# Kernel optimization log

Hardware: AMD Instinct MI355X
Metric: run time of the kernel (lower is better)

Reference implementation:

```python
import jax, jax.numpy as jnp
import numpy as np

B, N, C, D = 2, 6, 64, 40
FH, FW = 12, 33
IMG_H, IMG_W = 384, 1056
NX, NY, NZ = 100, 100, 4
LOWER = np.array([-50.0, -50.0, -10.0], np.float32)   # xbound[0], ybound[0], zbound[0]
DXV = np.array([1.0, 1.0, 5.0], np.float32)           # voxel sizes


def _conv(x, w, pad):
    return jax.lax.conv_general_dilated(x, w, (1, 1), [(pad, pad), (pad, pad)],
                                        dimension_numbers=('NCHW', 'OIHW', 'NCHW'))


def _bn(x, s, b):
    return x * s[None, :, None, None] + b[None, :, None, None]


def _se(x, w1, b1, w2, b2):
    m = x.mean((2, 3))                                   # global avg pool -> (B, C)
    g = jax.nn.sigmoid(jax.nn.silu(m @ w1.T + b1) @ w2.T + b2)
    return x * g[:, :, None, None]


def _frustum():
    ds = jnp.arange(4.0, 44.0, 1.0)                      # (D,) depth bins
    xs = jnp.linspace(0.0, IMG_W - 1.0, FW)
    ys = jnp.linspace(0.0, IMG_H - 1.0, FH)
    f = jnp.stack(jnp.broadcast_arrays(xs[None, None, :], ys[None, :, None], ds[:, None, None]), -1)
    return f.reshape(-1, 3)                              # (D*FH*FW, 3) in (x_px, y_px, depth)


def reference(feats, rots, trans, intrinsics, nw1, bn1s, bn1b, se1w1, se1b1, se1w2, se1b2,
              nw2, bn2s, bn2b, dhw, dhb, chw, chb, bcw1, bcs1, bcb1, bcsw1, bcsb1, bcsw2,
              bcsb2, bcw2, bcs2, bcb2, dw1, ds1, db1, dw2, db2):
    BN = B * N
    # ---- CamEncoderV2 neck + heads (backbone 1280ch@1/32 features given directly) ----
    x = jax.nn.silu(_bn(_conv(feats, nw1, 0), bn1s, bn1b))
    x = _se(x, se1w1, se1b1, se1w2, se1b2)
    x = jax.nn.silu(_bn(_conv(x, nw2, 1), bn2s, bn2b))
    depth = jax.nn.softmax(_conv(x, dhw, 0) + dhb[None, :, None, None], axis=1)  # (BN, D, FH, FW)
    ctx = _conv(x, chw, 0) + chb[None, :, None, None]                            # (BN, C, FH, FW)
    # ---- geometry: pixel frustum -> ego-frame points ----
    rots_f = rots.reshape(BN, 3, 3)
    trans_f = trans.reshape(BN, 3)
    K = intrinsics.reshape(BN, 3, 3)
    pts = _frustum()                                     # (P0, 3), P0 = D*FH*FW
    d = pts[:, 2]
    fx, fy = K[:, 0, 0][:, None], K[:, 1, 1][:, None]
    cx, cy = K[:, 0, 2][:, None], K[:, 1, 2][:, None]
    cam = jnp.stack([(pts[None, :, 0] - cx) * d[None, :] / fx,
                     (pts[None, :, 1] - cy) * d[None, :] / fy,
                     jnp.broadcast_to(d[None, :], (BN, d.shape[0]))], -1)        # (BN, P0, 3)
    geom = jnp.einsum('bij,bpj->bpi', rots_f, cam) + trans_f[:, None, :]
    geom = geom.reshape(B, -1, 3)                        # (B, N*P0, 3)
    # ---- lift: outer product context x depth ----
    ff = (ctx[:, None, :, :, :] * depth[:, :, None, :, :])                       # (BN, D, C, FH, FW)
    ff = ff.transpose(0, 1, 3, 4, 2).reshape(B, -1, C)                           # (B, N*P0, C)
    # ---- splat: voxel pooling (scatter-add into BEV grid) ----
    idx = jnp.floor((geom - jnp.asarray(LOWER)) / jnp.asarray(DXV)).astype(jnp.int32)
    valid = jnp.all((idx >= 0) & (idx < jnp.array([NX, NY, NZ])), axis=-1)
    sid = idx[..., 2] * (NX * NY) + idx[..., 0] * NY + idx[..., 1]
    sid = jnp.where(valid, sid, 0)
    ffm = ff * valid[..., None]
    pooled = jax.vmap(lambda f, i: jax.ops.segment_sum(f, i, num_segments=NZ * NX * NY))(ffm, sid)
    bev = pooled.reshape(B, NZ, NX, NY, C).transpose(0, 1, 4, 2, 3).reshape(B, NZ * C, NX, NY)
    # ---- BEVCompressorV2 (residual conv-SE-conv) ----
    h = jax.nn.relu(_bn(_conv(bev, bcw1, 1), bcs1, bcb1))
    h = _se(h, bcsw1, bcsb1, bcsw2, bcsb2)
    h = jax.nn.relu(_bn(_conv(h, bcw2, 1), bcs2, bcb2))
    bev = bev + h
    # ---- decoder ----
    h = jax.nn.relu(_bn(_conv(bev, dw1, 1), ds1, db1))
    out = _conv(h, dw2, 0) + db2[None, :, None, None]    # (B, nz*num_classes, NX, NY)
    return out.reshape(B, 4, NZ, NX, NY)


def setup_inputs():
    f32 = jnp.float32
    ks = jax.random.split(jax.random.key(0), 16)
    feats = jax.random.normal(ks[0], (B * N, 1280, FH, FW), f32) * 0.5
    # cam->ego: z_cam -> x_ego, -x_cam -> y_ego, -y_cam -> z_ego, plus per-camera yaw
    Rbase = np.array([[0., 0., 1.], [-1., 0., 0.], [0., -1., 0.]], np.float32)
    yaw = np.deg2rad(np.arange(N) * 60.0).astype(np.float32)
    c, s = np.cos(yaw), np.sin(yaw)
    Rz = np.zeros((N, 3, 3), np.float32)
    Rz[:, 0, 0] = c; Rz[:, 0, 1] = -s; Rz[:, 1, 0] = s; Rz[:, 1, 1] = c; Rz[:, 2, 2] = 1.0
    rots = jnp.asarray(np.broadcast_to(np.einsum('nij,jk->nik', Rz, Rbase), (B, N, 3, 3)).copy())
    trans = jax.random.normal(ks[1], (B, N, 3), f32) * 1.0
    K = np.array([[800., 0., 528.], [0., 800., 192.], [0., 0., 1.]], np.float32)
    intrinsics = jnp.asarray(np.broadcast_to(K, (B, N, 3, 3)).copy())

    def w(k, shape, fan_in):
        return jax.random.normal(k, shape, f32) * np.float32(np.sqrt(2.0 / fan_in))

    kk = jax.random.split(ks[2], 16)
    return dict(
        feats=feats, rots=rots, trans=trans, intrinsics=intrinsics,
        nw1=w(kk[0], (256, 1280, 1, 1), 1280), bn1s=jnp.ones(256, f32), bn1b=jnp.zeros(256, f32),
        se1w1=w(kk[1], (32, 256), 256), se1b1=jnp.zeros(32, f32),
        se1w2=w(kk[2], (256, 32), 32), se1b2=jnp.zeros(256, f32),
        nw2=w(kk[3], (256, 256, 3, 3), 2304), bn2s=jnp.ones(256, f32), bn2b=jnp.zeros(256, f32),
        dhw=w(kk[4], (40, 256, 1, 1), 256), dhb=jnp.zeros(40, f32),
        chw=w(kk[5], (64, 256, 1, 1), 256), chb=jnp.zeros(64, f32),
        bcw1=w(kk[6], (256, 256, 3, 3), 2304), bcs1=jnp.ones(256, f32), bcb1=jnp.zeros(256, f32),
        bcsw1=w(kk[7], (16, 256), 256), bcsb1=jnp.zeros(16, f32),
        bcsw2=w(kk[8], (256, 16), 16), bcsb2=jnp.zeros(256, f32),
        bcw2=w(kk[9], (256, 256, 3, 3), 2304), bcs2=jnp.ones(256, f32), bcb2=jnp.zeros(256, f32),
        dw1=w(kk[10], (128, 256, 3, 3), 2304), ds1=jnp.ones(128, f32), db1=jnp.zeros(128, f32),
        dw2=w(kk[11], (16, 128, 1, 1), 128), db2=jnp.zeros(16, f32),
    )
```

## Files before the change

kernel.cpp:

```cpp
#include <hip/hip_runtime.h>
#include <hip/hip_bf16.h>
#include <cmath>


typedef __attribute__((ext_vector_type(8))) short short8;
typedef __attribute__((ext_vector_type(4))) float floatx4;
typedef __hip_bfloat16 hb;

__device__ __forceinline__ float sigf(float x){ return 1.0f/(1.0f+expf(-x)); }
__device__ __forceinline__ float siluf(float x){ return x*sigf(x); }
__device__ __forceinline__ void split2(float v, hb* h, hb* l){
  hb hv = __float2bfloat16(v);
  *h = hv; *l = __float2bfloat16(v - __bfloat162float(hv));
}

__global__ __launch_bounds__(256) void k_trans_feats(
    const float* __restrict__ feats, hb* __restrict__ Fh, hb* __restrict__ Fl)
{
  __shared__ float tile[64][65];
  int n = blockIdx.z;
  int p0 = blockIdx.x*64;
  int c0 = blockIdx.y*64;
  int tid = threadIdx.x;
  int tr = tid >> 6;
  int tc = tid & 63;
  #pragma unroll
  for (int it=0; it<16; ++it){
    int ci = c0 + it*4 + tr;
    int p = p0 + tc;
    float v = 0.f;
    if (p < 396) v = feats[((size_t)n*1280 + ci)*396 + p];
    tile[it*4+tr][tc] = v;
  }
  __syncthreads();
  #pragma unroll
  for (int it=0; it<16; ++it){
    int pl = it*4 + tr;
    int p = p0 + pl;
    if (p < 396){
      hb hv, lv; split2(tile[tc][pl], &hv, &lv);
      size_t o = ((size_t)n*396 + p)*1280 + c0 + tc;
      Fh[o] = hv; Fl[o] = lv;
    }
  }
}

__global__ __launch_bounds__(256) void k_wpack1(
    const float* __restrict__ W, hb* __restrict__ Wph, hb* __restrict__ Wpl)
{
  int i = blockIdx.x*256 + threadIdx.x;
  if (i >= 40*16*512) return;
  int j = i & 7;
  int lane = (i>>3) & 63;
  int t2 = i >> 9;
  int nb = t2 & 15;
  int kb = t2 >> 4;
  int ci = kb*32 + (lane>>4)*8 + j;
  int co = nb*16 + (lane&15);
  hb hv, lv; split2(W[(size_t)co*1280 + ci], &hv, &lv);
  Wph[i] = hv; Wpl[i] = lv;
}

__global__ __launch_bounds__(256) void k_wpack(
    const float* __restrict__ W, hb* __restrict__ Wph, hb* __restrict__ Wpl, int NB)
{
  int i = blockIdx.x*256 + threadIdx.x;
  int total = 9*8*NB*512;
  if (i >= total) return;
  int j = i & 7;
  int t1 = i >> 3;
  int lane = t1 & 63;
  int t2 = t1 >> 6;
  int nb = t2 % NB;
  int t3 = t2 / NB;
  int kb = t3 & 7;
  int tap = t3 >> 3;
  int ci = kb*32 + (lane>>4)*8 + j;
  int co = nb*16 + (lane&15);
  hb hv, lv; split2(W[(size_t)co*2304 + ci*9 + tap], &hv, &lv);
  Wph[i] = hv; Wpl[i] = lv;
}

__global__ __launch_bounds__(256) void k_wpackT(
    const float* __restrict__ W, hb* __restrict__ Wph, hb* __restrict__ Wpl, int NB)
{
  int i = blockIdx.x*256 + threadIdx.x;
  int total = 9*8*NB*512;
  if (i >= total) return;
  int j = i & 7;
  int t1 = i >> 3;
  int lane = t1 & 63;
  int t2 = t1 >> 6;
  int nb = t2 % NB;
  int t3 = t2 / NB;
  int tap = t3 % 9;
  int kb = t3 / 9;
  int ci = kb*32 + (lane>>4)*8 + j;
  int co = nb*16 + (lane&15);
  hb hv, lv; split2(W[(size_t)co*2304 + ci*9 + tap], &hv, &lv);
  Wph[i] = hv; Wpl[i] = lv;
}

__global__ __launch_bounds__(256) void k_mfma_gemm1(
    const hb* __restrict__ Fh, const hb* __restrict__ Fl,
    const hb* __restrict__ Wph, const hb* __restrict__ Wpl,
    const float* __restrict__ bns, const float* __restrict__ bnb,
    float* __restrict__ out)
{
  __shared__ short8 lbh[256], lbl[256];
  int tid = threadIdx.x;
  int wv = tid >> 6, lane = tid & 63;
  int cog = blockIdx.y;
  int Pbase = blockIdx.x*128 + wv*32;
  int m = lane & 15, q = lane >> 4;
  int P0 = Pbase + m;      if (P0 > 4751) P0 = 4751;
  int P1 = Pbase + 16 + m; if (P1 > 4751) P1 = 4751;
  size_t rA0 = (size_t)P0*160 + q;
  size_t rA1 = (size_t)P1*160 + q;
  const short8* gAh = (const short8*)(const void*)Fh;
  const short8* gAl = (const short8*)(const void*)Fl;
  const short8* gWh = (const short8*)(const void*)Wph;
  const short8* gWl = (const short8*)(const void*)Wpl;
  size_t sb = (size_t)(cog*4 + wv)*64 + lane;
  floatx4 acc[2][4];
  #pragma unroll
  for (int i=0;i<2;++i)
    #pragma unroll
    for (int j=0;j<4;++j) acc[i][j] = (floatx4)(0.f);
  short8 ph = gWh[sb], pw = gWl[sb];
  short8 cah0 = gAh[rA0], cal0 = gAl[rA0], cah1 = gAh[rA1], cal1 = gAl[rA1];
  for (int kb=0; kb<40; ++kb){
    __syncthreads();
    lbh[tid] = ph; lbl[tid] = pw;
    int nx = (kb+1 < 40) ? kb+1 : 39;
    ph = gWh[(size_t)nx*1024 + sb]; pw = gWl[(size_t)nx*1024 + sb];
    __syncthreads();
    short8 nah0 = gAh[rA0 + (size_t)nx*4];
    short8 nal0 = gAl[rA0 + (size_t)nx*4];
    short8 nah1 = gAh[rA1 + (size_t)nx*4];
    short8 nal1 = gAl[rA1 + (size_t)nx*4];
    #pragma unroll
    for (int nb=0; nb<4; ++nb){
      short8 bh = lbh[nb*64 + lane];
      short8 bl = lbl[nb*64 + lane];
      acc[0][nb] = __builtin_amdgcn_mfma_f32_16x16x32_bf16(cah0, bh, acc[0][nb], 0,0,0);
      acc[0][nb] = __builtin_amdgcn_mfma_f32_16x16x32_bf16(cah0, bl, acc[0][nb], 0,0,0);
      acc[0][nb] = __builtin_amdgcn_mfma_f32_16x16x32_bf16(cal0, bh, acc[0][nb], 0,0,0);
      acc[1][nb] = __builtin_amdgcn_mfma_f32_16x16x32_bf16(cah1, bh, acc[1][nb], 0,0,0);
      acc[1][nb] = __builtin_amdgcn_mfma_f32_16x16x32_bf16(cah1, bl, acc[1][nb], 0,0,0);
      acc[1][nb] = __builtin_amdgcn_mfma_f32_16x16x32_bf16(cal1, bh, acc[1][nb], 0,0,0);
    }
    cah0 = nah0; cal0 = nal0; cah1 = nah1; cal1 = nal1;
  }
  int n16 = lane & 15;
  #pragma unroll
  for (int mg=0; mg<2; ++mg){
    #pragma unroll
    for (int nb=0; nb<4; ++nb){
      int co = cog*64 + nb*16 + n16;
      float s = bns[co], bv = bnb[co];
      #pragma unroll
      for (int r=0; r<4; ++r){
        int P = Pbase + mg*16 + q*4 + r;
        if (P < 4752) out[(size_t)P*256 + co] = siluf(acc[mg][nb][r]*s + bv);
      }
    }
  }
}

__global__ __launch_bounds__(256) void k_meanN(
    const float* __restrict__ x1, float* __restrict__ mean)
{
  int n = blockIdx.x; int c = threadIdx.x;
  float s = 0.f;
  for (int p=0; p<396; ++p) s += x1[((size_t)n*396+p)*256 + c];
  mean[n*256+c] = s*(1.f/396.f);
}

__global__ __launch_bounds__(256) void k_se_fc(
    const float* __restrict__ mean, const float* __restrict__ w1, const float* __restrict__ b1,
    const float* __restrict__ w2, const float* __restrict__ b2, float* __restrict__ g, int H)
{
  __shared__ float m[256];
  __shared__ float h[32];
  int n = blockIdx.x; int t = threadIdx.x;
  m[t] = mean[n*256 + t];
  __syncthreads();
  if (t < H){
    float s = b1[t];
    for (int c=0; c<256; ++c) s += m[c]*w1[t*256+c];
    h[t] = siluf(s);
  }
  __syncthreads();
  float s = b2[t];
  for (int j=0; j<H; ++j) s += h[j]*w2[t*H+j];
  g[n*256+t] = sigf(s);
}

__global__ __launch_bounds__(256) void k_topad(
    const float* __restrict__ x1, const float* __restrict__ g,
    hb* __restrict__ Xh, hb* __restrict__ Xl)
{
  int y = blockIdx.x;
  int n = blockIdx.y;
  int c = threadIdx.x;
  float gc = g[n*256+c];
  for (int xx=0; xx<35; ++xx){
    float v = 0.f;
    if (y>=1 && y<=12 && xx>=1 && xx<=33)
      v = x1[((size_t)n*396 + (y-1)*33 + (xx-1))*256 + c]*gc;
    hb hv, lv; split2(v, &hv, &lv);
    size_t o = (((size_t)n*14+y)*35+xx)*256 + c;
    Xh[o] = hv; Xl[o] = lv;
  }
}

__global__ __launch_bounds__(256) void k_conv3s_mfma(
    const hb* __restrict__ Xh, const hb* __restrict__ Xl,
    const hb* __restrict__ Wph, const hb* __restrict__ Wpl,
    const float* __restrict__ bns, const float* __restrict__ bnb,
    float* __restrict__ out)
{
  __shared__ short8 lbh[256], lbl[256];
  int tid = threadIdx.x;
  int wv = tid >> 6, lane = tid & 63;
  int cog = blockIdx.y;
  int Pbase = blockIdx.x*128 + wv*32;
  int m = lane & 15, q = lane >> 4;
  int P0 = Pbase + m;      if (P0 > 4751) P0 = 4751;
  int P1 = Pbase + 16 + m; if (P1 > 4751) P1 = 4751;
  int n0 = P0/396, pim0 = P0%396;
  int n1 = P1/396, pim1 = P1%396;
  size_t base0 = (size_t)((n0*14 + pim0/33)*35 + pim0%33)*32 + q;
  size_t base1 = (size_t)((n1*14 + pim1/33)*35 + pim1%33)*32 + q;
  const short8* gAh = (const short8*)(const void*)Xh;
  const short8* gAl = (const short8*)(const void*)Xl;
  const short8* gWh = (const short8*)(const void*)Wph;
  const short8* gWl = (const short8*)(const void*)Wpl;
  size_t sb = (size_t)(cog*4 + wv)*64 + lane;
  floatx4 acc[2][4];
  #pragma unroll
  for (int i=0;i<2;++i)
    #pragma unroll
    for (int j=0;j<4;++j) acc[i][j] = (floatx4)(0.f);
  short8 ph = gWh[sb], pw = gWl[sb];
  short8 cah0 = gAh[base0], cal0 = gAl[base0], cah1 = gAh[base1], cal1 = gAl[base1];
  for (int idx=0; idx<72; ++idx){
    __syncthreads();
    lbh[tid] = ph; lbl[tid] = pw;
    int nx = (idx+1 < 72) ? idx+1 : 71;
    ph = gWh[(size_t)nx*1024 + sb]; pw = gWl[(size_t)nx*1024 + sb];
    __syncthreads();
    int tap = nx >> 3, kb = nx & 7;
    int dy = (tap*11) >> 5;
    int dx = tap - dy*3;
    int ao = (dy*35+dx)*32 + kb*4;
    short8 nah0 = gAh[base0 + ao];
    short8 nal0 = gAl[base0 + ao];
    short8 nah1 = gAh[base1 + ao];
    short8 nal1 = gAl[base1 + ao];
    #pragma unroll
    for (int nb=0; nb<4; ++nb){
      short8 bh = lbh[nb*64 + lane];
      short8 bl = lbl[nb*64 + lane];
      acc[0][nb] = __builtin_amdgcn_mfma_f32_16x16x32_bf16(cah0, bh, acc[0][nb], 0,0,0);
      acc[0][nb] = __builtin_amdgcn_mfma_f32_16x16x32_bf16(cah0, bl, acc[0][nb], 0,0,0);
      acc[0][nb] = __builtin_amdgcn_mfma_f32_16x16x32_bf16(cal0, bh, acc[0][nb], 0,0,0);
      acc[1][nb] = __builtin_amdgcn_mfma_f32_16x16x32_bf16(cah1, bh, acc[1][nb], 0,0,0);
      acc[1][nb] = __builtin_amdgcn_mfma_f32_16x16x32_bf16(cah1, bl, acc[1][nb], 0,0,0);
      acc[1][nb] = __builtin_amdgcn_mfma_f32_16x16x32_bf16(cal1, bh, acc[1][nb], 0,0,0);
    }
    cah0 = nah0; cal0 = nal0; cah1 = nah1; cal1 = nal1;
  }
  int n16 = lane & 15;
  #pragma unroll
  for (int mg=0; mg<2; ++mg){
    #pragma unroll
    for (int r=0; r<4; ++r){
      int P = Pbase + mg*16 + q*4 + r;
      if (P < 4752){
        int nn = P/396, pim = P%396;
        #pragma unroll
        for (int nb=0; nb<4; ++nb){
          int co = cog*64 + nb*16 + n16;
          out[((size_t)nn*256+co)*396 + pim] = siluf(acc[mg][nb][r]*bns[co] + bnb[co]);
        }
      }
    }
  }
}

__global__ __launch_bounds__(256) void k_heads(
    const float* __restrict__ x, const float* __restrict__ dhw, const float* __restrict__ dhb,
    const float* __restrict__ chw, const float* __restrict__ chb,
    float* __restrict__ dep, float* __restrict__ ctx2)
{
  int p = blockIdx.x*256 + threadIdx.x;
  int co = blockIdx.y; int n = blockIdx.z;
  if (p >= 396) return;
  const float* xb = x + (size_t)n*256*396 + p;
  const float* w = (co < 40) ? (dhw + (size_t)co*256) : (chw + (size_t)(co-40)*256);
  float acc = 0.f;
  for (int ci=0; ci<256; ++ci) acc += xb[(size_t)ci*396] * w[ci];
  if (co < 40) dep[((size_t)n*40+co)*396 + p] = acc + dhb[co];
  else { int c = co-40; ctx2[((size_t)n*396+p)*64 + c] = acc + chb[c]; }
}

__global__ __launch_bounds__(256) void k_softmax40(float* __restrict__ dep)
{
  int i = blockIdx.x*256 + threadIdx.x;
  if (i >= 12*396) return;
  int n = i/396, p = i%396;
  float* base = dep + (size_t)n*40*396 + p;
  float mx = -1e30f;
  for (int d=0; d<40; ++d) mx = fmaxf(mx, base[(size_t)d*396]);
  float s = 0.f;
  for (int d=0; d<40; ++d){ float e = expf(base[(size_t)d*396]-mx); base[(size_t)d*396]=e; s+=e; }
  float inv = 1.f/s;
  for (int d=0; d<40; ++d) base[(size_t)d*396] *= inv;
}

__global__ __launch_bounds__(256) void k_geom(
    const float* __restrict__ rots, const float* __restrict__ trans,
    const float* __restrict__ intr, int* __restrict__ vox, int* __restrict__ cnt)
{
  int pt = blockIdx.x*256 + threadIdx.x;
  if (pt >= 190080) return;
  int b = pt/95040; int r = pt%95040;
  int n = r/15840;  int r2 = r%15840;
  int d = r2/396;   int pim = r2%396;
  int y = pim/33, x = pim%33;
  int bn = b*6+n;
  const float* R = rots + (size_t)bn*9;
  const float* T = trans + (size_t)bn*3;
  const float* K = intr + (size_t)bn*9;
  float fx=K[0], cx=K[2], fy=K[4], cy=K[5];
  float xs = (float)x * 32.96875f;
  float ys = (float)((double)y * (383.0/11.0));
  float dv = 4.0f + (float)d;
  float camx = (xs-cx)*dv/fx;
  float camy = (ys-cy)*dv/fy;
  float gx = R[0]*camx + R[1]*camy + R[2]*dv + T[0];
  float gy = R[3]*camx + R[4]*camy + R[5]*dv + T[1];
  float gz = R[6]*camx + R[7]*camy + R[8]*dv + T[2];
  int ix = (int)floorf(gx + 50.f);
  int iy = (int)floorf(gy + 50.f);
  int iz = (int)floorf((gz + 10.f)/5.f);
  bool valid = (ix>=0 && ix<100 && iy>=0 && iy<100 && iz>=0 && iz<4);
  int sid = iz*10000 + ix*100 + iy;
  vox[pt] = valid ? sid : -1;
  if (valid) atomicAdd(&cnt[b*40000 + sid], 1);
}

__global__ __launch_bounds__(256) void k_scan1(
    const int* __restrict__ cnt, int* __restrict__ off, int* __restrict__ bsum)
{
  __shared__ int s[256];
  int t = threadIdx.x;
  int i = blockIdx.x*256 + t;
  int v = (i < 80000) ? cnt[i] : 0;
  s[t] = v; __syncthreads();
  for (int o=1;o<256;o<<=1){
    int x = (t>=o) ? s[t-o] : 0;
    __syncthreads();
    s[t] += x;
    __syncthreads();
  }
  if (i < 80000) off[i] = s[t] - v;
  if (t == 255) bsum[blockIdx.x] = s[255];
}

__global__ void k_scan2(int* __restrict__ bsum, int nblk)
{
  if (threadIdx.x==0 && blockIdx.x==0){
    int run = 0;
    for (int j=0;j<nblk;++j){ int t = bsum[j]; bsum[j] = run; run += t; }
  }
}

__global__ __launch_bounds__(256) void k_scan3(
    int* __restrict__ off, const int* __restrict__ bsum, int* __restrict__ cur)
{
  int i = blockIdx.x*256 + threadIdx.x;
  if (i >= 80000) return;
  int o = off[i] + bsum[i>>8];
  off[i] = o;
  cur[i] = o;
}

__global__ __launch_bounds__(256) void k_fill(
    const int* __restrict__ vox, int* __restrict__ cur, int* __restrict__ list)
{
  int pt = blockIdx.x*256 + threadIdx.x;
  if (pt >= 190080) return;
  int s = vox[pt];
  if (s < 0) return;
  int b = pt/95040;
  int slot = atomicAdd(&cur[b*40000 + s], 1);
  list[slot] = pt;
}

__global__ __launch_bounds__(256) void k_gather(
    const int* __restrict__ off, const int* __restrict__ cnt, const int* __restrict__ list,
    const float* __restrict__ ctx2, const float* __restrict__ dep, float* __restrict__ bev)
{
  int tid = threadIdx.x;
  int bv = blockIdx.x*4 + (tid>>6);
  int c = tid & 63;
  int b = bv/40000, sid = bv%40000;
  int st = off[bv], nn = cnt[bv];
  float s = 0.f;
  for (int k=0;k<nn;++k){
    int pt = list[st+k];
    int r = pt%95040;
    int bn = b*6 + r/15840;
    int r2 = r%15840;
    int dd = r2/396, pim = r2%396;
    s += ctx2[((size_t)bn*396+pim)*64 + c] * dep[((size_t)bn*40+dd)*396 + pim];
  }
  int iz = sid/10000, rem = sid%10000;
  bev[(size_t)b*2560000 + (size_t)iz*640000 + (size_t)c*10000 + rem] = s;
}

__global__ __launch_bounds__(256) void k_tohwc2(
    const float* __restrict__ in, hb* __restrict__ Ah, hb* __restrict__ Al,
    const float* __restrict__ g)
{
  __shared__ float tile[32*105];
  int py = blockIdx.x;
  int b  = blockIdx.y;
  int cg = blockIdx.z;
  int tid = threadIdx.x;
  bool inner = (py >= 1 && py <= 100);
  if (inner){
    if (tid < 64){ int cil = tid & 31; int col = (tid>>5) ? 101 : 0; tile[cil*105 + col] = 0.f; }
    for (int i = tid; i < 3200; i += 256){
      int cil = i / 100, x = i % 100;
      int ci = cg*32 + cil;
      tile[cil*105 + (x+1)] = in[(((size_t)b*256 + ci)*100 + (py-1))*100 + x];
    }
  }
  __syncthreads();
  for (int i = tid; i < 32*102; i += 256){
    int px = i >> 5, cil = i & 31;
    int ci = cg*32 + cil;
    float v = 0.f;
    if (inner){
      v = tile[cil*105 + px];
      if (g) v *= g[b*256 + ci];
    }
    hb hv, lv; split2(v, &hv, &lv);
    size_t o = (((size_t)b*102 + py)*102 + px)*256 + ci;
    Ah[o] = hv; Al[o] = lv;
  }
}

__global__ __launch_bounds__(256) void k_rowmean(
    const float* __restrict__ in, float* __restrict__ out, int rowlen, float inv)
{
  __shared__ float ws[4];
  int row = blockIdx.x; int t = threadIdx.x;
  const float* p = in + (size_t)row*rowlen;
  float s = 0.f;
  for (int i=t; i<rowlen; i+=256) s += p[i];
  #pragma unroll
  for (int off=32; off; off>>=1) s += __shfl_down(s, off);
  if ((t&63)==0) ws[t>>6] = s;
  __syncthreads();
  if (t==0) out[row] = (ws[0]+ws[1]+ws[2]+ws[3]) * inv;
}

__global__ __launch_bounds__(256) void k_conv3_bevm(
    const hb* __restrict__ Ah, const hb* __restrict__ Al,
    const hb* __restrict__ Wph, const hb* __restrict__ Wpl,
    const float* __restrict__ bns, const float* __restrict__ bnb,
    const float* __restrict__ res, float* __restrict__ out, int Cout, int NBG)
{
  __shared__ __align__(16) short sAh[10*18*40];
  __shared__ __align__(16) short sAl[10*18*40];
  __shared__ short8 lbh[256], lbl[256];
  const int NB = Cout >> 4;
  int tid = threadIdx.x;
  int wv = tid >> 6, lane = tid & 63;
  int L = blockIdx.x;
  int spatial = L / (NBG*2);
  int rem = L % (NBG*2);
  int cog = rem % NBG;
  int bb  = rem / NBG;
  int xg = spatial % 7, yg = spatial / 7;
  int x0 = xg*16;
  int y0 = yg*8 + wv;
  int m = lane & 15, q = lane >> 4;
  int nb0 = cog*4;
  floatx4 acc[2][4];
  #pragma unroll
  for (int i=0;i<2;++i)
    #pragma unroll
    for (int j=0;j<4;++j) acc[i][j] = (floatx4)(0.f);

  const short8* gAh = (const short8*)(const void*)Ah;
  const short8* gAl = (const short8*)(const void*)Al;
  const short8* gWh = (const short8*)(const void*)Wph;
  const short8* gWl = (const short8*)(const void*)Wpl;
  const size_t nbstride = (size_t)NB*64;
  const size_t sb = (size_t)(nb0 + wv)*64 + lane;

  short8 ph = gWh[sb], pl = gWl[sb];

  for (int kb=0; kb<8; ++kb){
    #pragma unroll 3
    for (int tap=0; tap<9; ++tap){
      int idx2 = kb*9 + tap;
      __syncthreads();
      lbh[tid] = ph; lbl[tid] = pl;
      if (tap == 0){
        for (int i = tid; i < 720; i += 256){
          int rc = i >> 2, part = i & 3;
          int r = rc / 18, c = rc % 18;
          int yr = yg*8 + r; if (yr > 101) yr = 101;
          int xc = x0 + c;   if (xc > 101) xc = 101;
          size_t so = ((size_t)((bb*102 + yr)*102 + xc))*32 + kb*4 + part;
          short8 vh = gAh[so], vl = gAl[so];
          int dst = (r*18 + c)*40 + part*8;
          *(short8*)(sAh + dst) = vh;
          *(short8*)(sAl + dst) = vl;
        }
      }
      int nx = (idx2+1 < 72) ? idx2+1 : 71;
      ph = gWh[(size_t)nx*nbstride + sb];
      pl = gWl[(size_t)nx*nbstride + sb];
      __syncthreads();
      int dy = (tap*11) >> 5;
      int dx = tap - dy*3;
      int cc = dx + m;
      int a0 = ((wv + dy)*18 + cc)*40 + q*8;
      int a1 = ((wv + 4 + dy)*18 + cc)*40 + q*8;
      short8 cah0 = *(const short8*)(sAh + a0);
      short8 cal0 = *(const short8*)(sAl + a0);
      short8 cah1 = *(const short8*)(sAh + a1);
      short8 cal1 = *(const short8*)(sAl + a1);
      #pragma unroll
      for (int nb=0; nb<4; ++nb){
        short8 bh = lbh[nb*64 + lane];
        short8 bl = lbl[nb*64 + lane];
        acc[0][nb] = __builtin_amdgcn_mfma_f32_16x16x32_bf16(cah0, bh, acc[0][nb], 0,0,0);
        acc[0][nb] = __builtin_amdgcn_mfma_f32_16x16x32_bf16(cah0, bl, acc[0][nb], 0,0,0);
        acc[0][nb] = __builtin_amdgcn_mfma_f32_16x16x32_bf16(cal0, bh, acc[0][nb], 0,0,0);
        acc[1][nb] = __builtin_amdgcn_mfma_f32_16x16x32_bf16(cah1, bh, acc[1][nb], 0,0,0);
        acc[1][nb] = __builtin_amdgcn_mfma_f32_16x16x32_bf16(cah1, bl, acc[1][nb], 0,0,0);
        acc[1][nb] = __builtin_amdgcn_mfma_f32_16x16x32_bf16(cal1, bh, acc[1][nb], 0,0,0);
      }
    }
  }

  int n = lane & 15;
  int xq = x0 + q*4;
  #pragma unroll
  for (int mg=0; mg<2; ++mg){
    int yo = y0 + mg*4;
    if (yo < 100 && xq < 100){
      #pragma unroll
      for (int nb=0; nb<4; ++nb){
        int co = cog*64 + nb*16 + n;
        float s = bns[co], bv = bnb[co];
        floatx4 a = acc[mg][nb];
        float4 v;
        v.x = fmaxf(a[0]*s+bv, 0.f);
        v.y = fmaxf(a[1]*s+bv, 0.f);
        v.z = fmaxf(a[2]*s+bv, 0.f);
        v.w = fmaxf(a[3]*s+bv, 0.f);
        size_t o = ((size_t)(bb*Cout+co)*100 + yo)*100 + xq;
        if (res){
          float4 rv = *(const float4*)(res + o);
          v.x += rv.x; v.y += rv.y; v.z += rv.z; v.w += rv.w;
        }
        *(float4*)(out + o) = v;
      }
    }
  }
}

__global__ __launch_bounds__(256) void k_final(
    const float* __restrict__ h, const float* __restrict__ W, const float* __restrict__ bias,
    float* __restrict__ out)
{
  int pix = blockIdx.x*256 + threadIdx.x;
  int oc = blockIdx.y, b = blockIdx.z;
  if (pix >= 10000) return;
  const float* hb_ = h + (size_t)b*128*10000 + pix;
  const float* w = W + (size_t)oc*128;
  float acc = bias[oc];
  for (int ci=0; ci<128; ++ci) acc += hb_[(size_t)ci*10000]*w[ci];
  out[((size_t)(b*16+oc))*10000 + pix] = acc;
}

extern "C" void kernel_launch(void* const* d_in, const int* in_sizes, int n_in,
                              void* d_out, int out_size, void* d_ws, size_t ws_size,
                              hipStream_t stream)
{
  (void)in_sizes; (void)n_in; (void)out_size; (void)ws_size;
  const float* feats = (const float*)d_in[0];
  const float* rots  = (const float*)d_in[1];
  const float* trans = (const float*)d_in[2];
  const float* intr  = (const float*)d_in[3];
  const float* nw1   = (const float*)d_in[4];
  const float* bn1s  = (const float*)d_in[5];
  const float* bn1b  = (const float*)d_in[6];
  const float* se1w1 = (const float*)d_in[7];
  const float* se1b1 = (const float*)d_in[8];
  const float* se1w2 = (const float*)d_in[9];
  const float* se1b2 = (const float*)d_in[10];
  const float* nw2   = (const float*)d_in[11];
  const float* bn2s  = (const float*)d_in[12];
  const float* bn2b  = (const float*)d_in[13];
  const float* dhw   = (const float*)d_in[14];
  const float* dhb   = (const float*)d_in[15];
  const float* chw   = (const float*)d_in[16];
  const float* chb   = (const float*)d_in[17];
  const float* bcw1  = (const float*)d_in[18];
  const float* bcs1  = (const float*)d_in[19];
  const float* bcb1  = (const float*)d_in[20];
  const float* bcsw1 = (const float*)d_in[21];
  const float* bcsb1 = (const float*)d_in[22];
  const float* bcsw2 = (const float*)d_in[23];
  const float* bcsb2 = (const float*)d_in[24];
  const float* bcw2  = (const float*)d_in[25];
  const float* bcs2  = (const float*)d_in[26];
  const float* bcb2  = (const float*)d_in[27];
  const float* dw1   = (const float*)d_in[28];
  const float* ds1   = (const float*)d_in[29];
  const float* db1   = (const float*)d_in[30];
  const float* dw2   = (const float*)d_in[31];
  const float* db2   = (const float*)d_in[32];
  float* out = (float*)d_out;

  float* ws = (float*)d_ws;
  float* bev   = ws;
  float* h1    = ws + 5120000;
  hb*    Ah    = (hb*)(ws + 10240000);
  hb*    Al    = (hb*)(ws + 12903424);
  float* x2    = ws + 15566848;
  float* S5    = ws + 16783360;
  float* dep   = ws + 17373184;
  float* ctx2  = ws + 17563264;
  float* mean1 = ws + 17867392;
  float* g1    = mean1 + 3072;
  float* mean2 = g1 + 3072;
  float* g2    = mean2 + 512;
  int*   vox   = (int*)(ws + 17875584);
  hb* Fh   = (hb*)bev;
  hb* Wc1h = (hb*)(bev + 3041280);
  hb* Wc1l = (hb*)(bev + 3205120);
  float* x1 = h1;
  hb* Fl   = (hb*)(h1 + 1216512);
  hb* Xh   = (hb*)Ah;
  hb* Xl   = (hb*)Al;
  hb* Wc2h = (hb*)S5;
  hb* Wc2l = (hb*)(S5 + 294912);
  int* cnt  = (int*)h1;
  int* off  = cnt + 80000;
  int* cur  = off + 80000;
  int* bsum = cur + 80000;
  int* list = bsum + 1024;
  float* h3 = h1;
  hb* Wp1h = (hb*)x2;
  hb* Wp1l = (hb*)(x2 + 294912);
  hb* Wp3h = (hb*)(x2 + 589824);
  hb* Wp3l = (hb*)(x2 + 589824 + 147456);
  hb* Wp2h = (hb*)S5;
  hb* Wp2l = (hb*)(S5 + 294912);

  k_trans_feats<<<dim3(7,20,12),256,0,stream>>>(feats,Fh,Fl);
  k_wpack1<<<1280,256,0,stream>>>(nw1,Wc1h,Wc1l);
  k_mfma_gemm1<<<dim3(38,4),256,0,stream>>>(Fh,Fl,Wc1h,Wc1l,bn1s,bn1b,x1);
  k_meanN<<<12,256,0,stream>>>(x1,mean1);
  k_se_fc<<<12,256,0,stream>>>(mean1,se1w1,se1b1,se1w2,se1b2,g1,32);
  k_topad<<<dim3(14,12),256,0,stream>>>(x1,g1,Xh,Xl);
  k_wpack<<<(589824+255)/256,256,0,stream>>>(nw2,Wc2h,Wc2l,16);
  k_conv3s_mfma<<<dim3(38,4),256,0,stream>>>(Xh,Xl,Wc2h,Wc2l,bn2s,bn2b,x2);
  k_heads<<<dim3(2,104,12),256,0,stream>>>(x2,dhw,dhb,chw,chb,dep,ctx2);
  k_softmax40<<<(4752+255)/256,256,0,stream>>>(dep);

  k_wpackT<<<(589824+255)/256,256,0,stream>>>(bcw1,Wp1h,Wp1l,16);
  k_wpackT<<<(589824+255)/256,256,0,stream>>>(bcw2,Wp2h,Wp2l,16);
  k_wpackT<<<(294912+255)/256,256,0,stream>>>(dw1,Wp3h,Wp3l,8);

  hipMemsetAsync(cnt, 0, 80000*sizeof(int), stream);
  k_geom<<<(190080+255)/256,256,0,stream>>>(rots,trans,intr,vox,cnt);
  k_scan1<<<313,256,0,stream>>>(cnt,off,bsum);
  k_scan2<<<1,64,0,stream>>>(bsum,313);
  k_scan3<<<(80000+255)/256,256,0,stream>>>(off,bsum,cur);
  k_fill<<<(190080+255)/256,256,0,stream>>>(vox,cur,list);
  k_gather<<<20000,256,0,stream>>>(off,cnt,list,ctx2,dep,bev);

  k_tohwc2<<<dim3(102,2,8),256,0,stream>>>(bev,Ah,Al,nullptr);
  k_conv3_bevm<<<728,256,0,stream>>>(Ah,Al,Wp1h,Wp1l,bcs1,bcb1,nullptr,h1,256,4);
  k_rowmean<<<512,256,0,stream>>>(h1,mean2,10000,1e-4f);
  k_se_fc<<<2,256,0,stream>>>(mean2,bcsw1,bcsb1,bcsw2,bcsb2,g2,16);
  k_tohwc2<<<dim3(102,2,8),256,0,stream>>>(h1,Ah,Al,g2);
  k_conv3_bevm<<<728,256,0,stream>>>(Ah,Al,Wp2h,Wp2l,bcs2,bcb2,bev,bev,256,4);
  k_tohwc2<<<dim3(102,2,8),256,0,stream>>>(bev,Ah,Al,nullptr);
  k_conv3_bevm<<<364,256,0,stream>>>(Ah,Al,Wp3h,Wp3l,ds1,db1,nullptr,h3,128,2);
  k_final<<<dim3(40,16,2),256,0,stream>>>(h3,dw2,db2,out);
}
```

Baseline: 713.2 us.

## Fuse SE mean into GEMM, MFMA heads, double-buffer weight LDS, batch final conv

Several independent changes land together. The SE channel mean is accumulated with atomics inside the first GEMM epilogue, which removes the separate mean kernel. The 3x3 neck conv now writes split bf16 HWC output, so the depth and context heads can run as an MFMA GEMM with packed weights instead of a scalar per-channel loop. The BEV conv double-buffers its weight LDS slice and pads the activation tile stride to 44 to drop one barrier per tap and cut bank conflicts. The final 1x1 conv computes all 16 outputs per thread from shared weights. The atomics add contention and make the float summation order nondeterministic.

Measured after the change: 717.4 us. About the same (+0.6%).

```diff
diff --git a/kernel.cpp b/kernel.cpp
--- a/kernel.cpp
+++ b/kernel.cpp
@@ -101,11 +101,32 @@
   Wph[i] = hv; Wpl[i] = lv;
 }
 
+__global__ __launch_bounds__(256) void k_wpackH(
+    const float* __restrict__ dhw, const float* __restrict__ chw,
+    hb* __restrict__ Wph, hb* __restrict__ Wpl)
+{
+  int i = blockIdx.x*256 + threadIdx.x;
+  if (i >= 8*7*512) return;
+  int j = i & 7;
+  int t1 = i >> 3;
+  int lane = t1 & 63;
+  int t2 = t1 >> 6;
+  int nb = t2 % 7;
+  int kb = t2 / 7;
+  int ci = kb*32 + (lane>>4)*8 + j;
+  int co = nb*16 + (lane&15);
+  float w = 0.f;
+  if (co < 40) w = dhw[(size_t)co*256 + ci];
+  else if (co < 104) w = chw[(size_t)(co-40)*256 + ci];
+  hb hv, lv; split2(w, &hv, &lv);
+  Wph[i] = hv; Wpl[i] = lv;
+}
+
 __global__ __launch_bounds__(256) void k_mfma_gemm1(
     const hb* __restrict__ Fh, const hb* __restrict__ Fl,
     const hb* __restrict__ Wph, const hb* __restrict__ Wpl,
     const float* __restrict__ bns, const float* __restrict__ bnb,
-    float* __restrict__ out)
+    float* __restrict__ out, float* __restrict__ msum)
 {
   __shared__ short8 lbh[256], lbl[256];
   int tid = threadIdx.x;
@@ -162,29 +183,25 @@
       #pragma unroll
       for (int r=0; r<4; ++r){
         int P = Pbase + mg*16 + q*4 + r;
-        if (P < 4752) out[(size_t)P*256 + co] = siluf(acc[mg][nb][r]*s + bv);
+        if (P < 4752){
+          float v = siluf(acc[mg][nb][r]*s + bv);
+          out[(size_t)P*256 + co] = v;
+          atomicAdd(&msum[(P/396)*256 + co], v);
+        }
       }
     }
   }
-}
-
-__global__ __launch_bounds__(256) void k_meanN(
-    const float* __restrict__ x1, float* __restrict__ mean)
-{
-  int n = blockIdx.x; int c = threadIdx.x;
-  float s = 0.f;
-  for (int p=0; p<396; ++p) s += x1[((size_t)n*396+p)*256 + c];
-  mean[n*256+c] = s*(1.f/396.f);
 }
 
 __global__ __launch_bounds__(256) void k_se_fc(
     const float* __restrict__ mean, const float* __restrict__ w1, const float* __restrict__ b1,
-    const float* __restrict__ w2, const float* __restrict__ b2, float* __restrict__ g, int H)
+    const float* __restrict__ w2, const float* __restrict__ b2, float* __restrict__ g,
+    int H, float inv)
 {
   __shared__ float m[256];
   __shared__ float h[32];
   int n = blockIdx.x; int t = threadIdx.x;
-  m[t] = mean[n*256 + t];
+  m[t] = mean[n*256 + t] * inv;
   __syncthreads();
   if (t < H){
     float s = b1[t];
@@ -219,7 +236,7 @@
     const hb* __restrict__ Xh, const hb* __restrict__ Xl,
     const hb* __restrict__ Wph, const hb* __restrict__ Wpl,
     const float* __restrict__ bns, const float* __restrict__ bnb,
-    float* __restrict__ out)
+    hb* __restrict__ outh, hb* __restrict__ outl)
 {
   __shared__ short8 lbh[256], lbl[256];
   int tid = threadIdx.x;
@@ -279,31 +296,85 @@
     for (int r=0; r<4; ++r){
       int P = Pbase + mg*16 + q*4 + r;
       if (P < 4752){
-        int nn = P/396, pim = P%396;
         #pragma unroll
         for (int nb=0; nb<4; ++nb){
           int co = cog*64 + nb*16 + n16;
-          out[((size_t)nn*256+co)*396 + pim] = siluf(acc[mg][nb][r]*bns[co] + bnb[co]);
+          float v = siluf(acc[mg][nb][r]*bns[co] + bnb[co]);
+          hb hv, lv; split2(v, &hv, &lv);
+          outh[(size_t)P*256 + co] = hv;
+          outl[(size_t)P*256 + co] = lv;
         }
       }
     }
   }
 }
 
-__global__ __launch_bounds__(256) void k_heads(
-    const float* __restrict__ x, const float* __restrict__ dhw, const float* __restrict__ dhb,
-    const float* __restrict__ chw, const float* __restrict__ chb,
+__global__ __launch_bounds__(256) void k_headsM(
+    const hb* __restrict__ x2h, const hb* __restrict__ x2l,
+    const hb* __restrict__ Whh, const hb* __restrict__ Whl,
+    const float* __restrict__ dhb, const float* __restrict__ chb,
     float* __restrict__ dep, float* __restrict__ ctx2)
 {
-  int p = blockIdx.x*256 + threadIdx.x;
-  int co = blockIdx.y; int n = blockIdx.z;
-  if (p >= 396) return;
-  const float* xb = x + (size_t)n*256*396 + p;
-  const float* w = (co < 40) ? (dhw + (size_t)co*256) : (chw + (size_t)(co-40)*256);
-  float acc = 0.f;
-  for (int ci=0; ci<256; ++ci) acc += xb[(size_t)ci*396] * w[ci];
-  if (co < 40) dep[((size_t)n*40+co)*396 + p] = acc + dhb[co];
-  else { int c = co-40; ctx2[((size_t)n*396+p)*64 + c] = acc + chb[c]; }
+  __shared__ short8 lbh[256], lbl[256];
+  int tid = threadIdx.x;
+  int wv = tid >> 6, lane = tid & 63;
+  int cog = blockIdx.y;
+  int nb0 = cog*4;
+  int nbN = cog ? 3 : 4;
+  int Pbase = blockIdx.x*128 + wv*32;
+  int m = lane & 15, q = lane >> 4;
+  int P0 = Pbase + m;      if (P0 > 4751) P0 = 4751;
+  int P1 = Pbase + 16 + m; if (P1 > 4751) P1 = 4751;
+  size_t rA0 = (size_t)P0*32 + q;
+  size_t rA1 = (size_t)P1*32 + q;
+  const short8* gAh = (const short8*)(const void*)x2h;
+  const short8* gAl = (const short8*)(const void*)x2l;
+  const short8* gWh = (const short8*)(const void*)Whh;
+  const short8* gWl = (const short8*)(const void*)Whl;
+  floatx4 acc[2][4];
+  #pragma unroll
+  for (int i=0;i<2;++i)
+    #pragma unroll
+    for (int j=0;j<4;++j) acc[i][j] = (floatx4)(0.f);
+  for (int kb=0; kb<8; ++kb){
+    __syncthreads();
+    for (int i=tid; i<nbN*64; i+=256){
+      lbh[i] = gWh[(size_t)(kb*7 + nb0)*64 + i];
+      lbl[i] = gWl[(size_t)(kb*7 + nb0)*64 + i];
+    }
+    __syncthreads();
+    short8 ah0 = gAh[rA0 + kb*4], al0 = gAl[rA0 + kb*4];
+    short8 ah1 = gAh[rA1 + kb*4], al1 = gAl[rA1 + kb*4];
+    for (int nb=0; nb<nbN; ++nb){
+      short8 bh = lbh[nb*64 + lane];
+      short8 bl = lbl[nb*64 + lane];
+      acc[0][nb] = __builtin_amdgcn_mfma_f32_16x16x32_bf16(ah0, bh, acc[0][nb], 0,0,0);
+      acc[0][nb] = __builtin_amdgcn_mfma_f32_16x16x32_bf16(ah0, bl, acc[0][nb], 0,0,0);
+      acc[0][nb] = __builtin_amdgcn_mfma_f32_16x16x32_bf16(al0, bh, acc[0][nb], 0,0,0);
+      acc[1][nb] = __builtin_amdgcn_mfma_f32_16x16x32_bf16(ah1, bh, acc[1][nb], 0,0,0);
+      acc[1][nb] = __builtin_amdgcn_mfma_f32_16x16x32_bf16(ah1, bl, acc[1][nb], 0,0,0);
+      acc[1][nb] = __builtin_amdgcn_mfma_f32_16x16x32_bf16(al1, bh, acc[1][nb], 0,0,0);
+    }
+  }
+  int n16 = lane & 15;
+  #pragma unroll
+  for (int mg=0; mg<2; ++mg){
+    #pragma unroll
+    for (int r=0; r<4; ++r){
+      int P = Pbase + mg*16 + q*4 + r;
+      if (P < 4752){
+        int nn = P/396, pim = P%396;
+        for (int nb=0; nb<nbN; ++nb){
+          int co = cog*64 + nb*16 + n16;
+          float v = acc[mg][nb][r];
+          if (co < 40)
+            dep[((size_t)nn*40 + co)*396 + pim] = v + dhb[co];
+          else if (co < 104)
+            ctx2[((size_t)nn*396 + pim)*64 + (co-40)] = v + chb[co-40];
+        }
+      }
+    }
+  }
 }
 
 __global__ __launch_bounds__(256) void k_softmax40(float* __restrict__ dep)
@@ -476,9 +547,9 @@
     const float* __restrict__ bns, const float* __restrict__ bnb,
     const float* __restrict__ res, float* __restrict__ out, int Cout, int NBG)
 {
-  __shared__ __align__(16) short sAh[10*18*40];
-  __shared__ __align__(16) short sAl[10*18*40];
-  __shared__ short8 lbh[256], lbl[256];
+  __shared__ __align__(16) short sAh[10*18*44];
+  __shared__ __align__(16) short sAl[10*18*44];
+  __shared__ short8 lbh[2][256], lbl[2][256];
   const int NB = Cout >> 4;
   int tid = threadIdx.x;
   int wv = tid >> 6, lane = tid & 63;
@@ -506,14 +577,14 @@
   const size_t sb = (size_t)(nb0 + wv)*64 + lane;
 
   short8 ph = gWh[sb], pl = gWl[sb];
+  int cur = 0;
 
   for (int kb=0; kb<8; ++kb){
     #pragma unroll 3
     for (int tap=0; tap<9; ++tap){
       int idx2 = kb*9 + tap;
-      __syncthreads();
-      lbh[tid] = ph; lbl[tid] = pl;
       if (tap == 0){
+        __syncthreads();
         for (int i = tid; i < 720; i += 256){
           int rc = i >> 2, part = i & 3;
           int r = rc / 18, c = rc % 18;
@@ -521,11 +592,12 @@
           int xc = x0 + c;   if (xc > 101) xc = 101;
           size_t so = ((size_t)((bb*102 + yr)*102 + xc))*32 + kb*4 + part;
           short8 vh = gAh[so], vl = gAl[so];
-          int dst = (r*18 + c)*40 + part*8;
+          int dst = (r*18 + c)*44 + part*8;
           *(short8*)(sAh + dst) = vh;
           *(short8*)(sAl + dst) = vl;
         }
       }
+      lbh[cur][tid] = ph; lbl[cur][tid] = pl;
       int nx = (idx2+1 < 72) ? idx2+1 : 71;
       ph = gWh[(size_t)nx*nbstride + sb];
       pl = gWl[(size_t)nx*nbstride + sb];
@@ -533,16 +605,16 @@
       int dy = (tap*11) >> 5;
       int dx = tap - dy*3;
       int cc = dx + m;
-      int a0 = ((wv + dy)*18 + cc)*40 + q*8;
-      int a1 = ((wv + 4 + dy)*18 + cc)*40 + q*8;
+      int a0 = ((wv + dy)*18 + cc)*44 + q*8;
+      int a1 = ((wv + 4 + dy)*18 + cc)*44 + q*8;
       short8 cah0 = *(const short8*)(sAh + a0);
       short8 cal0 = *(const short8*)(sAl + a0);
       short8 cah1 = *(const short8*)(sAh + a1);
       short8 cal1 = *(const short8*)(sAl + a1);
       #pragma unroll
       for (int nb=0; nb<4; ++nb){
-        short8 bh = lbh[nb*64 + lane];
-        short8 bl = lbl[nb*64 + lane];
+        short8 bh = lbh[cur][nb*64 + lane];
+        short8 bl = lbl[cur][nb*64 + lane];
         acc[0][nb] = __builtin_amdgcn_mfma_f32_16x16x32_bf16(cah0, bh, acc[0][nb], 0,0,0);
         acc[0][nb] = __builtin_amdgcn_mfma_f32_16x16x32_bf16(cah0, bl, acc[0][nb], 0,0,0);
         acc[0][nb] = __builtin_amdgcn_mfma_f32_16x16x32_bf16(cal0, bh, acc[0][nb], 0,0,0);
@@ -550,6 +622,7 @@
         acc[1][nb] = __builtin_amdgcn_mfma_f32_16x16x32_bf16(cah1, bl, acc[1][nb], 0,0,0);
         acc[1][nb] = __builtin_amdgcn_mfma_f32_16x16x32_bf16(cal1, bh, acc[1][nb], 0,0,0);
       }
+      cur ^= 1;
     }
   }
 
@@ -580,18 +653,31 @@
   }
 }
 
-__global__ __launch_bounds__(256) void k_final(
+__global__ __launch_bounds__(256) void k_final2(
     const float* __restrict__ h, const float* __restrict__ W, const float* __restrict__ bias,
     float* __restrict__ out)
 {
-  int pix = blockIdx.x*256 + threadIdx.x;
-  int oc = blockIdx.y, b = blockIdx.z;
+  __shared__ float wsl[2048];
+  __shared__ float bs[16];
+  int tid = threadIdx.x;
+  int b = blockIdx.y;
+  for (int i=tid; i<2048; i+=256) wsl[i] = W[i];
+  if (tid < 16) bs[tid] = bias[tid];
+  __syncthreads();
+  int pix = blockIdx.x*256 + tid;
   if (pix >= 10000) return;
+  float acc[16];
+  #pragma unroll
+  for (int oc=0; oc<16; ++oc) acc[oc] = bs[oc];
   const float* hb_ = h + (size_t)b*128*10000 + pix;
-  const float* w = W + (size_t)oc*128;
-  float acc = bias[oc];
-  for (int ci=0; ci<128; ++ci) acc += hb_[(size_t)ci*10000]*w[ci];
-  out[((size_t)(b*16+oc))*10000 + pix] = acc;
+  for (int ci=0; ci<128; ++ci){
+    float hv = hb_[(size_t)ci*10000];
+    #pragma unroll
+    for (int oc=0; oc<16; ++oc) acc[oc] += hv * wsl[oc*128 + ci];
+  }
+  #pragma unroll
+  for (int oc=0; oc<16; ++oc)
+    out[((size_t)(b*16+oc))*10000 + pix] = acc[oc];
 }
 
 extern "C" void kernel_launch(void* const* d_in, const int* in_sizes, int n_in,
@@ -657,6 +743,10 @@
   hb* Xl   = (hb*)Al;
   hb* Wc2h = (hb*)S5;
   hb* Wc2l = (hb*)(S5 + 294912);
+  hb* x2h  = (hb*)x2;
+  hb* x2l  = (hb*)(x2 + 608256);
+  hb* Whh  = (hb*)S5;
+  hb* Whl  = (hb*)(S5 + 14336);
   int* cnt  = (int*)h1;
   int* off  = cnt + 80000;
   int* cur  = off + 80000;
@@ -670,20 +760,21 @@
   hb* Wp2h = (hb*)S5;
   hb* Wp2l = (hb*)(S5 + 294912);
 
+  hipMemsetAsync(mean1, 0, 3072*sizeof(float), stream);
   k_trans_feats<<<dim3(7,20,12),256,0,stream>>>(feats,Fh,Fl);
   k_wpack1<<<1280,256,0,stream>>>(nw1,Wc1h,Wc1l);
-  k_mfma_gemm1<<<dim3(38,4),256,0,stream>>>(Fh,Fl,Wc1h,Wc1l,bn1s,bn1b,x1);
-  k_meanN<<<12,256,0,stream>>>(x1,mean1);
-  k_se_fc<<<12,256,0,stream>>>(mean1,se1w1,se1b1,se1w2,se1b2,g1,32);
+  k_mfma_gemm1<<<dim3(38,4),256,0,stream>>>(Fh,Fl,Wc1h,Wc1l,bn1s,bn1b,x1,mean1);
+  k_se_fc<<<12,256,0,stream>>>(mean1,se1w1,se1b1,se1w2,se1b2,g1,32,1.f/396.f);
   k_topad<<<dim3(14,12),256,0,stream>>>(x1,g1,Xh,Xl);
-  k_wpack<<<(589824+255)/256,256,0,stream>>>(nw2,Wc2h,Wc2l,16);
-  k_conv3s_mfma<<<dim3(38,4),256,0,stream>>>(Xh,Xl,Wc2h,Wc2l,bn2s,bn2b,x2);
-  k_heads<<<dim3(2,104,12),256,0,stream>>>(x2,dhw,dhb,chw,chb,dep,ctx2);
-  k_softmax40<<<(4752+255)/256,256,0,stream>>>(dep);
-
-  k_wpackT<<<(589824+255)/256,256,0,stream>>>(bcw1,Wp1h,Wp1l,16);
-  k_wpackT<<<(589824+255)/256,256,0,stream>>>(bcw2,Wp2h,Wp2l,16);
-  k_wpackT<<<(294912+255)/256,256,0,stream>>>(dw1,Wp3h,Wp3l,8);
+  k_wpack<<<2304,256,0,stream>>>(nw2,Wc2h,Wc2l,16);
+  k_conv3s_mfma<<<dim3(38,4),256,0,stream>>>(Xh,Xl,Wc2h,Wc2l,bn2s,bn2b,x2h,x2l);
+  k_wpackH<<<112,256,0,stream>>>(dhw,chw,Whh,Whl);
+  k_headsM<<<dim3(38,2),256,0,stream>>>(x2h,x2l,Whh,Whl,dhb,chb,dep,ctx2);
+  k_softmax40<<<19,256,0,stream>>>(dep);
+
+  k_wpackT<<<2304,256,0,stream>>>(bcw1,Wp1h,Wp1l,16);
+  k_wpackT<<<2304,256,0,stream>>>(bcw2,Wp2h,Wp2l,16);
+  k_wpackT<<<1152,256,0,stream>>>(dw1,Wp3h,Wp3l,8);
 
   hipMemsetAsync(cnt, 0, 80000*sizeof(int), stream);
   k_geom<<<(190080+255)/256,256,0,stream>>>(rots,trans,intr,vox,cnt);
@@ -696,10 +787,10 @@
   k_tohwc2<<<dim3(102,2,8),256,0,stream>>>(bev,Ah,Al,nullptr);
   k_conv3_bevm<<<728,256,0,stream>>>(Ah,Al,Wp1h,Wp1l,bcs1,bcb1,nullptr,h1,256,4);
   k_rowmean<<<512,256,0,stream>>>(h1,mean2,10000,1e-4f);
-  k_se_fc<<<2,256,0,stream>>>(mean2,bcsw1,bcsb1,bcsw2,bcsb2,g2,16);
+  k_se_fc<<<2,256,0,stream>>>(mean2,bcsw1,bcsb1,bcsw2,bcsb2,g2,16,1.f);
   k_tohwc2<<<dim3(102,2,8),256,0,stream>>>(h1,Ah,Al,g2);
   k_conv3_bevm<<<728,256,0,stream>>>(Ah,Al,Wp2h,Wp2l,bcs2,bcb2,bev,bev,256,4);
   k_tohwc2<<<dim3(102,2,8),256,0,stream>>>(bev,Ah,Al,nullptr);
   k_conv3_bevm<<<364,256,0,stream>>>(Ah,Al,Wp3h,Wp3l,ds1,db1,nullptr,h3,128,2);
-  k_final<<<dim3(40,16,2),256,0,stream>>>(h3,dw2,db2,out);
-}
+  k_final2<<<dim3(40,2),256,0,stream>>>(h3,dw2,db2,out);
+}
```
